# Kernel optimization log

Hardware: AMD Instinct MI355X
Metric: run time of the kernel (lower is better)

## Reference

```python
import jax, jax.numpy as jnp
import numpy as np

U = 100000   # num_users
I = 50000    # num_items
N = U + I    # total nodes
D = 64       # embed_size
L = 3        # n_layers
E = 2000000  # num edges
EPS = 1e-12  # F.normalize default eps


def setup_inputs() -> dict:
    key = jax.random.key(0)
    k1, k2, k3, k4 = jax.random.split(key, 4)
    user_emb = jax.random.normal(k1, (U, D), dtype=jnp.float32) * 0.1
    item_emb = jax.random.normal(k2, (I, D), dtype=jnp.float32) * 0.1
    rows = jax.random.randint(k3, (E,), 0, N, dtype=jnp.int32)
    cols = jax.random.randint(k4, (E,), 0, N, dtype=jnp.int32)
    return {"user_emb": user_emb, "item_emb": item_emb, "rows": rows, "cols": cols}


def _spmm(vals, rows, cols, x):
    # sparse [N,N] @ dense [N,D] via gather + segment reduce
    return jax.ops.segment_sum(vals[:, None] * x[cols], rows, num_segments=N)


def _l2norm(x):
    return x / jnp.maximum(jnp.linalg.norm(x, axis=1, keepdims=True), EPS)


def reference(user_emb, item_emb, rows, cols):
    emb0 = jnp.concatenate([user_emb, item_emb], axis=0)  # [N, D]

    # laplacian_adj: G = D^-1/2 A D^-1/2 on the same edge set
    deg = jax.ops.segment_sum(jnp.ones((E,), emb0.dtype), rows, num_segments=N)
    d_is = jnp.where(deg > 0, deg ** -0.5, 0.0)
    g_vals = d_is[rows] * d_is[cols]  # [E]

    cur = emb0
    acc = emb0
    user_fine, item_fine = [], []
    for _ in range(L):
        gnn = _spmm(g_vals, rows, cols, cur)  # [N, D]
        # fine_laplacian_adj: cosine-sim edge scores, row-normalized
        gr = _l2norm(gnn[rows])
        gc = _l2norm(gnn[cols])
        scores = (jnp.sum(gr * gc, axis=1) + 1.0) * 0.5  # [E] in [0,1]
        rowsum = jax.ops.segment_sum(scores, rows, num_segments=N)
        d_inv = jnp.where(rowsum > 0, 1.0 / rowsum, 0.0)
        fine = _spmm(d_inv[rows] * scores, rows, cols, cur)  # [N, D]
        cur = gnn + fine
        acc = acc + cur
        user_fine.append(fine[:U])
        item_fine.append(fine[U:])

    u_embs = acc[:U]
    i_embs = acc[U:]
    return (u_embs, i_embs, jnp.stack(user_fine, 0), jnp.stack(item_fine, 0))
```

## Files before the change

### kernel.cpp

```cpp
#include <hip/hip_runtime.h>

namespace {

typedef unsigned short u16;
typedef __attribute__((__ext_vector_type__(2))) float f32x2;
typedef __attribute__((__ext_vector_type__(4))) float f32x4;

constexpr int Un = 100000;
constexpr int In = 50000;
constexpr int Nn = 150000;
constexpr int D  = 64;
constexpr int Ln = 3;
constexpr int En = 2000000;
constexpr int CHUNK = 1024;
constexpr int NB = (Nn + CHUNK - 1) / CHUNK;
constexpr int DCAP = 128;
constexpr int NW = Nn / 8;

__device__ __forceinline__ u16 f2bf(float f) {
    unsigned u = __float_as_uint(f);
    unsigned r = (u + 0x7FFFu + ((u >> 16) & 1u)) >> 16;
    return (u16)r;
}
__device__ __forceinline__ float bflo(unsigned u) {
    return __uint_as_float(u << 16);
}
__device__ __forceinline__ float bfhi(unsigned u) {
    return __uint_as_float(u & 0xFFFF0000u);
}
__device__ __forceinline__ unsigned pack2(float lo, float hi) {
    return (unsigned)f2bf(lo) | ((unsigned)f2bf(hi) << 16);
}

__device__ __forceinline__ f32x2 pkfma(f32x2 a, f32x2 b, f32x2 c) {
    f32x2 d;
    asm("v_pk_fma_f32 %0, %1, %2, %3" : "=v"(d) : "v"(a), "v"(b), "v"(c));
    return d;
}
__device__ __forceinline__ f32x2 pkadd(f32x2 a, f32x2 b) {
    f32x2 d;
    asm("v_pk_add_f32 %0, %1, %2" : "=v"(d) : "v"(a), "v"(b));
    return d;
}

__device__ __forceinline__ float dpp_add8(float x) {
    x += __uint_as_float((unsigned)__builtin_amdgcn_update_dpp(
        0, (int)__float_as_uint(x), 0xB1, 0xF, 0xF, true));
    x += __uint_as_float((unsigned)__builtin_amdgcn_update_dpp(
        0, (int)__float_as_uint(x), 0x4E, 0xF, 0xF, true));
    x += __uint_as_float((unsigned)__builtin_amdgcn_update_dpp(
        0, (int)__float_as_uint(x), 0x141, 0xF, 0xF, true));
    return x;
}

__device__ __forceinline__ void unp8(uint4 q, f32x2* o) {
    o[0].x = bflo(q.x); o[0].y = bfhi(q.x);
    o[1].x = bflo(q.y); o[1].y = bfhi(q.y);
    o[2].x = bflo(q.z); o[2].y = bfhi(q.z);
    o[3].x = bflo(q.w); o[3].y = bfhi(q.w);
}

__global__ void count_kernel(const int* __restrict__ rows, int* __restrict__ deg,
                             int* __restrict__ eoff) {
    int e = blockIdx.x * blockDim.x + threadIdx.x;
    if (e < En) eoff[e] = atomicAdd(&deg[rows[e]], 1);
}

__global__ void scan_partial(const int* __restrict__ deg, float* __restrict__ d_is,
                             int* __restrict__ bsum) {
    int tid = threadIdx.x;
    int base = blockIdx.x * CHUNK + tid * 4;
    int s = 0;
#pragma unroll
    for (int i = 0; i < 4; ++i) {
        int idx = base + i;
        if (idx < Nn) {
            int d = deg[idx];
            s += d;
            d_is[idx] = d > 0 ? rsqrtf((float)d) : 0.f;
        }
    }
    __shared__ int sh[256];
    sh[tid] = s;
    __syncthreads();
    for (int o = 128; o > 0; o >>= 1) {
        if (tid < o) sh[tid] += sh[tid + o];
        __syncthreads();
    }
    if (tid == 0) bsum[blockIdx.x] = sh[0];
}

__global__ void scan_top(int* __restrict__ bsum, int* __restrict__ row_ptr) {
    __shared__ int sh[256];
    int tid = threadIdx.x;
    int v = (tid < NB) ? bsum[tid] : 0;
    sh[tid] = v;
    __syncthreads();
    for (int o = 1; o < 256; o <<= 1) {
        int t = (tid >= o) ? sh[tid - o] : 0;
        __syncthreads();
        sh[tid] += t;
        __syncthreads();
    }
    if (tid < NB) bsum[tid] = sh[tid] - v;
    if (tid == 255) row_ptr[Nn] = sh[255];
}

__global__ void scan_final(const int* __restrict__ deg, const int* __restrict__ bsum,
                           int* __restrict__ row_ptr) {
    int tid = threadIdx.x;
    int base = blockIdx.x * CHUNK + tid * 4;
    int v[4];
    int ts = 0;
#pragma unroll
    for (int i = 0; i < 4; ++i) {
        int idx = base + i;
        v[i] = (idx < Nn) ? deg[idx] : 0;
        ts += v[i];
    }
    __shared__ int sh[256];
    sh[tid] = ts;
    __syncthreads();
    for (int o = 1; o < 256; o <<= 1) {
        int t = (tid >= o) ? sh[tid - o] : 0;
        __syncthreads();
        sh[tid] += t;
        __syncthreads();
    }
    int excl = bsum[blockIdx.x] + sh[tid] - ts;
#pragma unroll
    for (int i = 0; i < 4; ++i) {
        int idx = base + i;
        if (idx < Nn) row_ptr[idx] = excl;
        excl += v[i];
    }
}

__global__ void fill_kernel(const int* __restrict__ rows, const int* __restrict__ cols,
                            const int* __restrict__ row_ptr, const int* __restrict__ eoff,
                            int* __restrict__ col_off) {
    int e = blockIdx.x * blockDim.x + threadIdx.x;
    if (e >= En) return;
    col_off[row_ptr[rows[e]] + eoff[e]] = cols[e] << 7;
}

__global__ void hist_part(const int* __restrict__ deg, int* __restrict__ hp) {
    __shared__ int lh[DCAP];
    int tid = threadIdx.x;
    if (tid < DCAP) lh[tid] = 0;
    __syncthreads();
    int base = blockIdx.x * CHUNK + tid * 4;
#pragma unroll
    for (int i = 0; i < 4; ++i) {
        int idx = base + i;
        if (idx < Nn) atomicAdd(&lh[min(deg[idx], DCAP - 1)], 1);
    }
    __syncthreads();
    if (tid < DCAP) hp[tid * NB + blockIdx.x] = lh[tid];
}

__global__ void hp_scan(int* __restrict__ hp) {
    constexpr int TOT = DCAP * NB;
    constexpr int PER = (TOT + 1023) / 1024;
    __shared__ int sh[1024];
    int tid = threadIdx.x;
    int base = tid * PER;
    int s = 0;
    for (int i = 0; i < PER; ++i) {
        int idx = base + i;
        if (idx < TOT) s += hp[idx];
    }
    sh[tid] = s;
    __syncthreads();
    for (int o = 1; o < 1024; o <<= 1) {
        int t = (tid >= o) ? sh[tid - o] : 0;
        __syncthreads();
        sh[tid] += t;
        __syncthreads();
    }
    int excl = sh[tid] - s;
    for (int i = 0; i < PER; ++i) {
        int idx = base + i;
        if (idx < TOT) {
            int v = hp[idx];
            hp[idx] = excl;
            excl += v;
        }
    }
}

__global__ void perm_scatter(const int* __restrict__ deg, const int* __restrict__ row_ptr,
                             const float* __restrict__ d_is, const int* __restrict__ hp,
                             int4* __restrict__ srt) {
    __shared__ int lh[DCAP];
    __shared__ int lbase[DCAP];
    int tid = threadIdx.x;
    if (tid < DCAP) lh[tid] = 0;
    __syncthreads();
    int base = blockIdx.x * CHUNK + tid * 4;
    int bin[4], rank[4];
#pragma unroll
    for (int i = 0; i < 4; ++i) {
        int idx = base + i;
        if (idx < Nn) {
            bin[i] = min(deg[idx], DCAP - 1);
            rank[i] = atomicAdd(&lh[bin[i]], 1);
        }
    }
    __syncthreads();
    if (tid < DCAP) lbase[tid] = hp[tid * NB + blockIdx.x];
    __syncthreads();
#pragma unroll
    for (int i = 0; i < 4; ++i) {
        int idx = base + i;
        if (idx < Nn) {
            int p = lbase[bin[i]] + rank[i];
            int4 v;
            v.x = row_ptr[idx];
            v.y = row_ptr[idx + 1];
            v.z = __float_as_int(d_is[idx]);
            v.w = idx;
            srt[p] = v;
        }
    }
}

__global__ void init_kernel(const float* __restrict__ ue, const float* __restrict__ ie,
                            const float* __restrict__ d_is,
                            float* __restrict__ out, u16* __restrict__ cur,
                            u16* __restrict__ S) {
    int i = (blockIdx.x * 256 + threadIdx.x) * 4;
    if (i >= Nn * D) return;
    const float* src = (i < Un * D) ? (ue + i) : (ie + (i - Un * D));
    float4 v = *(const float4*)src;
    *(float4*)(out + i) = v;
    ushort4 q;
    q.x = f2bf(v.x); q.y = f2bf(v.y); q.z = f2bf(v.z); q.w = f2bf(v.w);
    *(ushort4*)(cur + i) = q;
    float ds = d_is[i >> 6];
    ushort4 qs;
    qs.x = f2bf(v.x * ds); qs.y = f2bf(v.y * ds);
    qs.z = f2bf(v.z * ds); qs.w = f2bf(v.w * ds);
    *(ushort4*)(S + i) = qs;
}

__global__ __launch_bounds__(256) void spmm_gnn(const u16* __restrict__ S_,
                                                u16* __restrict__ Qn_,
                                                const int4* __restrict__ srt,
                                                const int* __restrict__ col_off,
                                                float* __restrict__ normv_s) {
    int w = (blockIdx.x * 256 + threadIdx.x) >> 6;
    if (w >= NW) return;
    int lane = threadIdx.x & 63;
    int g = lane >> 3, l = lane & 7;
    unsigned l16 = (unsigned)l * 16u;
    int wb = w * 8 + g;
    int4 q4 = srt[wb];
    int s = q4.x, t = q4.y;
    float dr = __int_as_float(q4.z);
    int r = q4.w;
    const char* pS = (const char*)S_;
    f32x2 z; z.x = 0.f; z.y = 0.f;
    f32x2 a2[4] = {z, z, z, z};
#pragma unroll 4
    for (int j = s; j < t; ++j) {
        unsigned off = (unsigned)col_off[j];
        uint4 q = *(const uint4*)(pS + (off + l16));
        f32x2 x2[4];
        unp8(q, x2);
#pragma unroll
        for (int p = 0; p < 4; ++p) a2[p] = pkadd(a2[p], x2[p]);
    }
    float sq = 0.f;
#pragma unroll
    for (int p = 0; p < 4; ++p) {
        sq = fmaf(a2[p].x, a2[p].x, sq);
        sq = fmaf(a2[p].y, a2[p].y, sq);
    }
    sq = dpp_add8(sq);
    float gn = dr * sqrtf(sq);
    float nrm = fmaxf(gn, 1e-12f);
    float scale = dr / nrm;
    if (l == 0) normv_s[wb] = nrm;
    unsigned ro = ((unsigned)r << 7) + l16;
    uint4 on;
    on.x = pack2(a2[0].x * scale, a2[0].y * scale);
    on.y = pack2(a2[1].x * scale, a2[1].y * scale);
    on.z = pack2(a2[2].x * scale, a2[2].y * scale);
    on.w = pack2(a2[3].x * scale, a2[3].y * scale);
    *(uint4*)((char*)Qn_ + ro) = on;
}

__global__ __launch_bounds__(256) void score_fine_kernel(const u16* __restrict__ A_,
                                                         const u16* __restrict__ Qn_,
                                                         u16* __restrict__ C_,
                                                         u16* __restrict__ S_,
                                                         const float* __restrict__ normv_s,
                                                         const int4* __restrict__ srt,
                                                         const int* __restrict__ col_off,
                                                         float* __restrict__ out, int layer) {
    int w = (blockIdx.x * 256 + threadIdx.x) >> 6;
    if (w >= NW) return;
    int lane = threadIdx.x & 63;
    int g = lane >> 3, l = lane & 7;
    unsigned l16 = (unsigned)l * 16u;
    int wb = w * 8 + g;
    int4 q4 = srt[wb];
    int s = q4.x, t = q4.y;
    float dsr = __int_as_float(q4.z);
    int r = q4.w;
    float nrm = normv_s[wb];
    const char* pQn = (const char*)Qn_;
    const char* pA  = (const char*)A_;
    unsigned ro = ((unsigned)r << 7) + l16;
    uint4 qbn = *(const uint4*)(pQn + ro);
    f32x2 b2[4];
    unp8(qbn, b2);
    f32x2 z; z.x = 0.f; z.y = 0.f;
    f32x2 facc[4] = {z, z, z, z};
    float rowsum = 0.f;
#pragma unroll 2
    for (int j = s; j < t; ++j) {
        unsigned off = (unsigned)col_off[j];
        unsigned vo = off + l16;
        uint4 qx = *(const uint4*)(pQn + vo);
        uint4 qy = *(const uint4*)(pA + vo);
        f32x2 x2[4];
        unp8(qx, x2);
        f32x2 d2 = pkfma(b2[0], x2[0], z);
        d2 = pkfma(b2[1], x2[1], d2);
        d2 = pkfma(b2[2], x2[2], d2);
        d2 = pkfma(b2[3], x2[3], d2);
        float d = dpp_add8(d2.x + d2.y);
        float sc = fmaf(d, 0.5f, 0.5f);
        rowsum += sc;
        f32x2 y2[4];
        unp8(qy, y2);
        f32x2 sc2; sc2.x = sc; sc2.y = sc;
#pragma unroll
        for (int p = 0; p < 4; ++p) facc[p] = pkfma(sc2, y2[p], facc[p]);
    }
    float di = rowsum > 0.f ? 1.f / rowsum : 0.f;
    float f[8] = {facc[0].x * di, facc[0].y * di, facc[1].x * di, facc[1].y * di,
                  facc[2].x * di, facc[2].y * di, facc[3].x * di, facc[3].y * di};
    float bb[8] = {b2[0].x, b2[0].y, b2[1].x, b2[1].y,
                   b2[2].x, b2[2].y, b2[3].x, b2[3].y};
    float cn[8];
#pragma unroll
    for (int k = 0; k < 8; ++k) cn[k] = fmaf(bb[k], nrm, f[k]);
    uint4 qn;
    qn.x = pack2(cn[0], cn[1]); qn.y = pack2(cn[2], cn[3]);
    qn.z = pack2(cn[4], cn[5]); qn.w = pack2(cn[6], cn[7]);
    *(uint4*)((char*)C_ + ro) = qn;
    if (layer != Ln - 1) {
        uint4 qs;
        qs.x = pack2(cn[0] * dsr, cn[1] * dsr);
        qs.y = pack2(cn[2] * dsr, cn[3] * dsr);
        qs.z = pack2(cn[4] * dsr, cn[5] * dsr);
        qs.w = pack2(cn[6] * dsr, cn[7] * dsr);
        *(uint4*)((char*)S_ + ro) = qs;
    }
    float* op = out + (size_t)r * D + l * 8;
    float4 a0 = ((float4*)op)[0], a1 = ((float4*)op)[1];
    a0.x += cn[0]; a0.y += cn[1]; a0.z += cn[2]; a0.w += cn[3];
    a1.x += cn[4]; a1.y += cn[5]; a1.z += cn[6]; a1.w += cn[7];
    ((float4*)op)[0] = a0;
    ((float4*)op)[1] = a1;
    size_t fo;
    if (r < Un)
        fo = (size_t)Nn * D + (size_t)layer * Un * D + (size_t)r * D + l * 8;
    else
        fo = (size_t)Nn * D + (size_t)Ln * Un * D + (size_t)layer * In * D
             + (size_t)(r - Un) * D + l * 8;
    f32x4 f0, f1;
    f0.x = f[0]; f0.y = f[1]; f0.z = f[2]; f0.w = f[3];
    f1.x = f[4]; f1.y = f[5]; f1.z = f[6]; f1.w = f[7];
    __builtin_nontemporal_store(f0, (f32x4*)(out + fo));
    __builtin_nontemporal_store(f1, (f32x4*)(out + fo) + 1);
}

}

extern "C" void kernel_launch(void* const* d_in, const int* in_sizes, int n_in,
                              void* d_out, int out_size, void* d_ws, size_t ws_size,
                              hipStream_t stream) {
    const float* user_emb = (const float*)d_in[0];
    const float* item_emb = (const float*)d_in[1];
    const int* rows = (const int*)d_in[2];
    const int* cols = (const int*)d_in[3];
    float* out = (float*)d_out;

    char* ws = (char*)d_ws;
    size_t off = 0;
    auto alloc = [&](size_t bytes) -> void* {
        void* p = ws + off;
        off += (bytes + 255) & ~size_t(255);
        return p;
    };
    u16*   buf0    = (u16*)  alloc((size_t)Nn * D * 2);
    u16*   buf1    = (u16*)  alloc((size_t)Nn * D * 2);
    u16*   buf2    = (u16*)  alloc((size_t)Nn * D * 2);
    u16*   buf3    = (u16*)  alloc((size_t)Nn * D * 2);
    int*   col_off = (int*)  alloc((size_t)(En + 8) * 4);
    int*   deg     = (int*)  alloc((size_t)Nn * 4);
    int*   row_ptr = (int*)  alloc((size_t)(Nn + 1) * 4);
    float* d_is    = (float*)alloc((size_t)Nn * 4);
    float* normv_s = (float*)alloc((size_t)Nn * 4);
    int4*  srt     = (int4*) alloc((size_t)Nn * 16);
    int*   hp      = (int*)  alloc((size_t)DCAP * NB * 4);
    int*   bsum    = (int*)  alloc(4096);
    int*   eoff    = (int*)buf2;
    (void)ws_size; (void)in_sizes; (void)n_in; (void)out_size;

    hipMemsetAsync(deg, 0, (size_t)Nn * 4, stream);

    const int EB = (En + 255) / 256;
    count_kernel<<<EB, 256, 0, stream>>>(rows, deg, eoff);
    scan_partial<<<NB, 256, 0, stream>>>(deg, d_is, bsum);
    scan_top<<<1, 256, 0, stream>>>(bsum, row_ptr);
    scan_final<<<NB, 256, 0, stream>>>(deg, bsum, row_ptr);
    hist_part<<<NB, 256, 0, stream>>>(deg, hp);
    hp_scan<<<1, 1024, 0, stream>>>(hp);
    fill_kernel<<<EB, 256, 0, stream>>>(rows, cols, row_ptr, eoff, col_off);
    perm_scatter<<<NB, 256, 0, stream>>>(deg, row_ptr, d_is, hp, srt);
    init_kernel<<<(Nn * D / 4 + 255) / 256, 256, 0, stream>>>(user_emb, item_emb, d_is,
                                                              out, buf0, buf3);

    const int WB = (NW * 64 + 255) / 256;
    u16* P = buf0;
    u16* R = buf1;
    u16* Qn = buf2;
    u16* S  = buf3;
    for (int l = 0; l < Ln; ++l) {
        spmm_gnn<<<WB, 256, 0, stream>>>(S, Qn, srt, col_off, normv_s);
        score_fine_kernel<<<WB, 256, 0, stream>>>(P, Qn, R, S, normv_s, srt,
                                                  col_off, out, l);
        u16* tmp = P; P = R; R = tmp;
    }
}
```

Measured before the change: 810.4 us.

## Replace global degree sort with per-block local sort, widen init, raise unrolls

Removes the global degree histogram and its single-block scan kernel, so the node permutation is now sorted by degree only within each 1024-node chunk using a block-local prefix scan. The init kernel handles 8 elements per thread and packs pairs to bf16. The unroll factors of both SpMM loops are raised. Only local sorting may give worse wave load balance across chunks, and it saves two launches including a serial single-block scan.

After: 824.1 us. About the same (+1.7%).

```diff
diff --git a/kernel.cpp b/kernel.cpp
--- a/kernel.cpp
+++ b/kernel.cpp
@@ -144,56 +144,10 @@
     col_off[row_ptr[rows[e]] + eoff[e]] = cols[e] << 7;
 }
 
-__global__ void hist_part(const int* __restrict__ deg, int* __restrict__ hp) {
+__global__ void perm_scatter(const int* __restrict__ deg, const int* __restrict__ row_ptr,
+                             const float* __restrict__ d_is, int4* __restrict__ srt) {
     __shared__ int lh[DCAP];
-    int tid = threadIdx.x;
-    if (tid < DCAP) lh[tid] = 0;
-    __syncthreads();
-    int base = blockIdx.x * CHUNK + tid * 4;
-#pragma unroll
-    for (int i = 0; i < 4; ++i) {
-        int idx = base + i;
-        if (idx < Nn) atomicAdd(&lh[min(deg[idx], DCAP - 1)], 1);
-    }
-    __syncthreads();
-    if (tid < DCAP) hp[tid * NB + blockIdx.x] = lh[tid];
-}
-
-__global__ void hp_scan(int* __restrict__ hp) {
-    constexpr int TOT = DCAP * NB;
-    constexpr int PER = (TOT + 1023) / 1024;
-    __shared__ int sh[1024];
-    int tid = threadIdx.x;
-    int base = tid * PER;
-    int s = 0;
-    for (int i = 0; i < PER; ++i) {
-        int idx = base + i;
-        if (idx < TOT) s += hp[idx];
-    }
-    sh[tid] = s;
-    __syncthreads();
-    for (int o = 1; o < 1024; o <<= 1) {
-        int t = (tid >= o) ? sh[tid - o] : 0;
-        __syncthreads();
-        sh[tid] += t;
-        __syncthreads();
-    }
-    int excl = sh[tid] - s;
-    for (int i = 0; i < PER; ++i) {
-        int idx = base + i;
-        if (idx < TOT) {
-            int v = hp[idx];
-            hp[idx] = excl;
-            excl += v;
-        }
-    }
-}
-
-__global__ void perm_scatter(const int* __restrict__ deg, const int* __restrict__ row_ptr,
-                             const float* __restrict__ d_is, const int* __restrict__ hp,
-                             int4* __restrict__ srt) {
-    __shared__ int lh[DCAP];
-    __shared__ int lbase[DCAP];
+    __shared__ int sc[DCAP];
     int tid = threadIdx.x;
     if (tid < DCAP) lh[tid] = 0;
     __syncthreads();
@@ -208,13 +162,21 @@
         }
     }
     __syncthreads();
-    if (tid < DCAP) lbase[tid] = hp[tid * NB + blockIdx.x];
+    if (tid < DCAP) sc[tid] = lh[tid];
+    __syncthreads();
+    for (int o = 1; o < DCAP; o <<= 1) {
+        int t = (tid < DCAP && tid >= o) ? sc[tid - o] : 0;
+        __syncthreads();
+        if (tid < DCAP) sc[tid] += t;
+        __syncthreads();
+    }
+    if (tid < DCAP) sc[tid] -= lh[tid];
     __syncthreads();
 #pragma unroll
     for (int i = 0; i < 4; ++i) {
         int idx = base + i;
         if (idx < Nn) {
-            int p = lbase[bin[i]] + rank[i];
+            int p = blockIdx.x * CHUNK + sc[bin[i]] + rank[i];
             int4 v;
             v.x = row_ptr[idx];
             v.y = row_ptr[idx + 1];
@@ -229,19 +191,22 @@
                             const float* __restrict__ d_is,
                             float* __restrict__ out, u16* __restrict__ cur,
                             u16* __restrict__ S) {
-    int i = (blockIdx.x * 256 + threadIdx.x) * 4;
-    if (i >= Nn * D) return;
-    const float* src = (i < Un * D) ? (ue + i) : (ie + (i - Un * D));
-    float4 v = *(const float4*)src;
-    *(float4*)(out + i) = v;
-    ushort4 q;
-    q.x = f2bf(v.x); q.y = f2bf(v.y); q.z = f2bf(v.z); q.w = f2bf(v.w);
-    *(ushort4*)(cur + i) = q;
-    float ds = d_is[i >> 6];
-    ushort4 qs;
-    qs.x = f2bf(v.x * ds); qs.y = f2bf(v.y * ds);
-    qs.z = f2bf(v.z * ds); qs.w = f2bf(v.w * ds);
-    *(ushort4*)(S + i) = qs;
+    int i8 = (blockIdx.x * 256 + threadIdx.x) * 8;
+    if (i8 >= Nn * D) return;
+    const float* src = (i8 < Un * D) ? (ue + i8) : (ie + (i8 - Un * D));
+    float4 v0 = ((const float4*)src)[0];
+    float4 v1 = ((const float4*)src)[1];
+    ((float4*)(out + i8))[0] = v0;
+    ((float4*)(out + i8))[1] = v1;
+    uint4 qc;
+    qc.x = pack2(v0.x, v0.y); qc.y = pack2(v0.z, v0.w);
+    qc.z = pack2(v1.x, v1.y); qc.w = pack2(v1.z, v1.w);
+    *(uint4*)((char*)cur + (size_t)i8 * 2) = qc;
+    float ds = d_is[i8 >> 6];
+    uint4 qs;
+    qs.x = pack2(v0.x * ds, v0.y * ds); qs.y = pack2(v0.z * ds, v0.w * ds);
+    qs.z = pack2(v1.x * ds, v1.y * ds); qs.w = pack2(v1.z * ds, v1.w * ds);
+    *(uint4*)((char*)S + (size_t)i8 * 2) = qs;
 }
 
 __global__ __launch_bounds__(256) void spmm_gnn(const u16* __restrict__ S_,
@@ -262,7 +227,7 @@
     const char* pS = (const char*)S_;
     f32x2 z; z.x = 0.f; z.y = 0.f;
     f32x2 a2[4] = {z, z, z, z};
-#pragma unroll 4
+#pragma unroll 8
     for (int j = s; j < t; ++j) {
         unsigned off = (unsigned)col_off[j];
         uint4 q = *(const uint4*)(pS + (off + l16));
@@ -319,7 +284,7 @@
     f32x2 z; z.x = 0.f; z.y = 0.f;
     f32x2 facc[4] = {z, z, z, z};
     float rowsum = 0.f;
-#pragma unroll 2
+#pragma unroll 4
     for (int j = s; j < t; ++j) {
         unsigned off = (unsigned)col_off[j];
         unsigned vo = off + l16;
@@ -407,7 +372,6 @@
     float* d_is    = (float*)alloc((size_t)Nn * 4);
     float* normv_s = (float*)alloc((size_t)Nn * 4);
     int4*  srt     = (int4*) alloc((size_t)Nn * 16);
-    int*   hp      = (int*)  alloc((size_t)DCAP * NB * 4);
     int*   bsum    = (int*)  alloc(4096);
     int*   eoff    = (int*)buf2;
     (void)ws_size; (void)in_sizes; (void)n_in; (void)out_size;
@@ -419,11 +383,9 @@
     scan_partial<<<NB, 256, 0, stream>>>(deg, d_is, bsum);
     scan_top<<<1, 256, 0, stream>>>(bsum, row_ptr);
     scan_final<<<NB, 256, 0, stream>>>(deg, bsum, row_ptr);
-    hist_part<<<NB, 256, 0, stream>>>(deg, hp);
-    hp_scan<<<1, 1024, 0, stream>>>(hp);
     fill_kernel<<<EB, 256, 0, stream>>>(rows, cols, row_ptr, eoff, col_off);
-    perm_scatter<<<NB, 256, 0, stream>>>(deg, row_ptr, d_is, hp, srt);
-    init_kernel<<<(Nn * D / 4 + 255) / 256, 256, 0, stream>>>(user_emb, item_emb, d_is,
+    perm_scatter<<<NB, 256, 0, stream>>>(deg, row_ptr, d_is, srt);
+    init_kernel<<<(Nn * D / 8 + 255) / 256, 256, 0, stream>>>(user_emb, item_emb, d_is,
                                                               out, buf0, buf3);
 
     const int WB = (NW * 64 + 255) / 256;
```
